# Optimization experiments

Measured on AMD Instinct MI355X. Metric: run time of the kernel, lower is better.

The kernel has to match this reference:

```python
import jax, jax.numpy as jnp
import numpy as np

N, IN_DIM, OUT_DIM, HEADS = 2048, 512, 512, 8
HEAD_DIM = OUT_DIM // HEADS
NEG_SLOPE = 0.2


def setup_inputs() -> dict:
    key = jax.random.key(0)
    k1, k2, k3, k4 = jax.random.split(key, 4)
    x = jax.random.normal(k1, (N, IN_DIM), dtype=jnp.float32)
    adj = jax.random.randint(k2, (N, N), 0, 2, dtype=jnp.int32)
    W = jax.random.normal(k3, (IN_DIM, OUT_DIM), dtype=jnp.float32) * 0.02
    a = jax.random.normal(k4, (2 * HEAD_DIM,), dtype=jnp.float32) * 0.02
    return {"x": x, "adj": adj, "W": W, "a": a}


def reference(x, adj, W, a):
    # Wh: (N, H, Dh)
    Wh = (x @ W).reshape(N, HEADS, HEAD_DIM)
    # a . concat(Wh_i, Wh_j) == (Wh_i . a_src) + (Wh_j . a_dst) -- exact decomposition,
    # avoids materializing the (N, N, H, 2*Dh) concat tensor.
    a_src, a_dst = a[:HEAD_DIM], a[HEAD_DIM:]
    s_i = jnp.einsum('nhd,d->nh', Wh, a_src)  # contribution of dest node i
    s_j = jnp.einsum('nhd,d->nh', Wh, a_dst)  # contribution of source node j
    e = jax.nn.leaky_relu(s_i[:, None, :] + s_j[None, :, :], negative_slope=NEG_SLOPE)  # (N, N, H)
    mask = (adj > 0)[:, :, None]
    e = jnp.where(mask, e, jnp.float32(-jnp.inf))
    alpha = jax.nn.softmax(e, axis=1)  # softmax over source nodes j
    # out[i,h,:] = sum_j alpha[i,j,h] * Wh[j,h,:]   (dropout is identity at eval)
    out = jnp.einsum('ijh,jhd->ihd', alpha, Wh)
    return out.reshape(N, OUT_DIM)
```

## Files before the change

kernel.cpp:

```cpp
#include <hip/hip_runtime.h>
#include <hip/hip_bf16.h>

#define NN 2048
#define KD 512
#define ODIM 512
#define NHEAD 8
#define HD 64
#define NEG 0.2f

typedef float f32x4 __attribute__((ext_vector_type(4)));
typedef short bf16x8 __attribute__((ext_vector_type(8)));
typedef short bf16x4 __attribute__((ext_vector_type(4)));
typedef unsigned long long u64;
typedef unsigned int u32;

__device__ __forceinline__ short tob(float f) {
  __hip_bfloat16 h = __float2bfloat16(f);
  return *reinterpret_cast<short*>(&h);
}

__device__ __forceinline__ void gl_lds16(const void* g, void* l) {
  __builtin_amdgcn_global_load_lds(
      (const __attribute__((address_space(1))) u32*)g,
      (__attribute__((address_space(3))) u32*)l, 16, 0, 0);
}
__device__ __forceinline__ void gl_lds4(const void* g, void* l) {
  __builtin_amdgcn_global_load_lds(
      (const __attribute__((address_space(1))) u32*)g,
      (__attribute__((address_space(3))) u32*)l, 4, 0, 0);
}

__global__ __launch_bounds__(256) void prep(const float* __restrict__ X,
                                            const float* __restrict__ W,
                                            const int* __restrict__ adj,
                                            short* __restrict__ Xf,
                                            short* __restrict__ Bf,
                                            unsigned short* __restrict__ bits) {
  __shared__ float sbuf[16 * 516];
  const int b = blockIdx.x;
  const int t = threadIdx.x;

  if (b < 1024) {
    const int T = b * 256 + t;
    const int row = T >> 7, g = T & 127;
    const int* p = adj + (size_t)row * NN + g * 16;
    u32 m = 0;
#pragma unroll
    for (int q = 0; q < 4; ++q) {
      const int4 v = *(const int4*)&p[q * 4];
      m |= (v.x > 0 ? 1u : 0u) << (q * 4);
      m |= (v.y > 0 ? 2u : 0u) << (q * 4);
      m |= (v.z > 0 ? 4u : 0u) << (q * 4);
      m |= (v.w > 0 ? 8u : 0u) << (q * 4);
    }
    bits[T] = (unsigned short)m;
    return;
  }

  if (b < 1024 + 128) {
    const int xb = b - 1024;
#pragma unroll
    for (int q = 0; q < 8; ++q) {
      const int flat = q * 256 + t;
      const int row = flat >> 7, c4 = flat & 127;
      const float4 v = *(const float4*)&X[(size_t)(xb * 16 + row) * KD + c4 * 4];
      *(float4*)&sbuf[row * 516 + c4 * 4] = v;
    }
    __syncthreads();
#pragma unroll
    for (int c = 0; c < 4; ++c) {
      const int s = c * 256 + t;
      const int ks = s >> 6, l = s & 63;
      const int col = l & 15, kg = (l >> 4) & 3;
      const int k0 = ks * 32 + kg * 8;
      bf16x8 o;
#pragma unroll
      for (int u = 0; u < 8; ++u) o[u] = tob(sbuf[col * 516 + k0 + u]);
      *(bf16x8*)&Xf[((size_t)xb * 1024 + s) * 8] = o;
    }
    return;
  }

  const int b2 = b - 1152;
  const int kb = b2 & 7, h = b2 >> 3;
  const int k0 = kb * 64;
#pragma unroll
  for (int q = 0; q < 4; ++q) {
    const int flat = q * 256 + t;
    const int kk = flat >> 4, o4 = (flat & 15) * 4;
    const float4 v = *(const float4*)&W[(size_t)(k0 + kk) * ODIM + h * 64 + o4];
    *(float4*)&sbuf[kk * 68 + o4] = v;
  }
  __syncthreads();
#pragma unroll
  for (int c = 0; c < 2; ++c) {
    const int s = c * 256 + t;
    const int ksl = s >> 8, nt = (s >> 6) & 3, l = s & 63;
    const int col = l & 15, kg = (l >> 4) & 3;
    const int kloc = ksl * 32 + kg * 8;
    const int od = nt * 16 + col;
    bf16x8 o;
#pragma unroll
    for (int u = 0; u < 8; ++u) o[u] = tob(sbuf[(kloc + u) * 68 + od]);
    const size_t off = (((size_t)(h * 4 + nt) * 16 + kb * 2 + ksl) * 64 + l) * 8;
    *(bf16x8*)&Bf[off] = o;
  }
}

__global__ __launch_bounds__(256) void gemm_fused(
    const short* __restrict__ Xf, const short* __restrict__ Bf,
    const float* __restrict__ a, short* __restrict__ WhF,
    float2* __restrict__ esrcp, u32* __restrict__ edstp) {
  const int t = threadIdx.x;
  const int lane = t & 63, w = t >> 6;
  const int col = lane & 15, kgrp = lane >> 4;
  const int bm = blockIdx.x * 64;
  const int h = blockIdx.y;
  const int mt = blockIdx.x * 4 + w;

  const short* ax = Xf + (size_t)mt * 8192;
  const short* bx = Bf + (size_t)h * 32768;

  f32x4 acc[4] = {};

#pragma unroll
  for (int ks = 0; ks < 16; ++ks) {
    const bf16x8 af = *(const bf16x8*)&ax[(ks * 64 + lane) * 8];
#pragma unroll
    for (int nt = 0; nt < 4; ++nt) {
      const bf16x8 bf = *(const bf16x8*)&bx[((nt * 16 + ks) * 64 + lane) * 8];
      acc[nt] = __builtin_amdgcn_mfma_f32_16x16x32_bf16(af, bf, acc[nt], 0, 0, 0);
    }
  }

  float asv[4], adv[4];
#pragma unroll
  for (int nt = 0; nt < 4; ++nt) {
    asv[nt] = a[nt * 16 + col];
    adv[nt] = a[64 + nt * 16 + col];
  }
  float ps[4], pd[4];
#pragma unroll
  for (int r = 0; r < 4; ++r) {
    float s1 = 0.f, s2 = 0.f;
#pragma unroll
    for (int nt = 0; nt < 4; ++nt) {
      s1 += acc[nt][r] * asv[nt];
      s2 += acc[nt][r] * adv[nt];
    }
    ps[r] = s1;
    pd[r] = s2;
  }
#pragma unroll
  for (int off = 1; off <= 8; off <<= 1) {
#pragma unroll
    for (int r = 0; r < 4; ++r) {
      ps[r] += __shfl_xor(ps[r], off);
      pd[r] += __shfl_xor(pd[r], off);
    }
  }
  {
    const size_t tbase = ((size_t)h * 32 + blockIdx.x) * 4096;
    const int lp = ((w & 1) * 2 + (kgrp >> 1)) * 16 + col;
    const int u0 = (kgrp & 1) * 4;
    const int slot_ks = w >> 1;
#pragma unroll
    for (int nt = 0; nt < 4; ++nt) {
      bf16x4 o;
#pragma unroll
      for (int r = 0; r < 4; ++r) o[r] = tob(acc[nt][r]);
      *(bf16x4*)&WhF[tbase + (size_t)(nt * 2 + slot_ks) * 512 + lp * 8 + u0] = o;
    }
  }
  if (col == 0) {
    const int mbase = bm + w * 16 + kgrp * 4;
#pragma unroll
    for (int r = 0; r < 4; ++r) {
      const int n = mbase + r;
      esrcp[h * NN + n] = make_float2(__expf(ps[r]), __expf(NEG * ps[r]));
      const u32 lo = (u32)(unsigned short)tob(__expf(pd[r]));
      const u32 hi = (u32)(unsigned short)tob(__expf(NEG * pd[r]));
      edstp[h * NN + n] = (hi << 16) | lo;
    }
  }
}

__global__ __launch_bounds__(256) void attn_mfma(
    const short* __restrict__ WhF, const unsigned char* __restrict__ adjbits,
    const float2* __restrict__ esrcp, const u32* __restrict__ edstp,
    float* __restrict__ out) {
  extern __shared__ __align__(16) char smem[];
  const int t = threadIdx.x;
  const int lane = t & 63;
  const int jq = t >> 6;
  const int col = lane & 15, kgrp = lane >> 4;
  const int h = blockIdx.y;
  const int i0 = blockIdx.x * 32;
  char* wbase = smem + jq * 17408;

  const short* tb = WhF + ((size_t)h * 32 + jq * 8) * 4096;
  const int jb = jq * 512;
  const int jboff = jb >> 3;

  const float2 e0 = esrcp[h * NN + i0 + col];
  const float2 e1 = esrcp[h * NN + i0 + 16 + col];
  const float A0 = e0.x, C0 = e0.y, A1 = e1.x, C1 = e1.y;

  bf16x8 ones;
#pragma unroll
  for (int u = 0; u < 8; ++u) ones[u] = (short)0x3F80;

  f32x4 acc[2][4] = {};
  f32x4 accd[2] = {};

  {
    char* bb = wbase;
#pragma unroll
    for (int s = 0; s < 8; ++s)
      gl_lds16(tb + s * 512 + lane * 8, bb + s * 1024);
    gl_lds4(edstp + h * NN + jb + lane, bb + 8192);
    gl_lds4(adjbits + (size_t)(i0 + (lane >> 1)) * 256 + jboff + (lane & 1) * 4,
            bb + 8448);
  }

#pragma unroll
  for (int tt = 0; tt < 8; ++tt) {
    char* bcur = wbase + (tt & 1) * 8704;
    char* bnxt = wbase + ((tt + 1) & 1) * 8704;
    if (tt < 7) {
      const short* g = tb + (size_t)(tt + 1) * 4096;
#pragma unroll
      for (int s = 0; s < 8; ++s)
        gl_lds16(g + s * 512 + lane * 8, bnxt + s * 1024);
      gl_lds4(edstp + h * NN + jb + (tt + 1) * 64 + lane, bnxt + 8192);
      gl_lds4(adjbits + (size_t)(i0 + (lane >> 1)) * 256 + jboff +
                  (tt + 1) * 8 + (lane & 1) * 4,
              bnxt + 8448);
      asm volatile("s_waitcnt vmcnt(10)" ::: "memory");
    } else {
      asm volatile("s_waitcnt vmcnt(0)" ::: "memory");
    }
    __builtin_amdgcn_sched_barrier(0);

    const u32* elds = (const u32*)(bcur + 8192);
    const u64 m0 = *(const u64*)(bcur + 8448 + col * 8);
    const u64 m1 = *(const u64*)(bcur + 8448 + 128 + col * 8);
    bf16x8 af0[2], af1[2];
#pragma unroll
    for (int ks = 0; ks < 2; ++ks) {
      const uint4 q0 = *(const uint4*)&elds[ks * 32 + kgrp * 8];
      const uint4 q1 = *(const uint4*)&elds[ks * 32 + kgrp * 8 + 4];
      const u32 mb0 = (u32)(m0 >> ((ks * 4 + kgrp) * 8)) & 0xffu;
      const u32 mb1 = (u32)(m1 >> ((ks * 4 + kgrp) * 8)) & 0xffu;
      const u32 uw[8] = {q0.x, q0.y, q0.z, q0.w, q1.x, q1.y, q1.z, q1.w};
#pragma unroll
      for (int u2 = 0; u2 < 8; ++u2) {
        const float B = __uint_as_float(uw[u2] << 16);
        const float D = __uint_as_float(uw[u2] & 0xffff0000u);
        float p0 = fmaxf(A0 * B, C0 * D);
        float p1 = fmaxf(A1 * B, C1 * D);
        p0 = ((mb0 >> u2) & 1u) ? p0 : 0.f;
        p1 = ((mb1 >> u2) & 1u) ? p1 : 0.f;
        af0[ks][u2] = tob(p0);
        af1[ks][u2] = tob(p1);
      }
    }

    const short* sb = (const short*)bcur;
    __builtin_amdgcn_s_setprio(1);
    accd[0] = __builtin_amdgcn_mfma_f32_16x16x32_bf16(af0[0], ones, accd[0], 0, 0, 0);
    accd[0] = __builtin_amdgcn_mfma_f32_16x16x32_bf16(af0[1], ones, accd[0], 0, 0, 0);
    accd[1] = __builtin_amdgcn_mfma_f32_16x16x32_bf16(af1[0], ones, accd[1], 0, 0, 0);
    accd[1] = __builtin_amdgcn_mfma_f32_16x16x32_bf16(af1[1], ones, accd[1], 0, 0, 0);
#pragma unroll
    for (int nt = 0; nt < 4; ++nt) {
      const bf16x8 b0 = *(const bf16x8*)&sb[(nt * 2 + 0) * 512 + lane * 8];
      const bf16x8 b1 = *(const bf16x8*)&sb[(nt * 2 + 1) * 512 + lane * 8];
      acc[0][nt] = __builtin_amdgcn_mfma_f32_16x16x32_bf16(af0[0], b0, acc[0][nt], 0, 0, 0);
      acc[1][nt] = __builtin_amdgcn_mfma_f32_16x16x32_bf16(af1[0], b0, acc[1][nt], 0, 0, 0);
      acc[0][nt] = __builtin_amdgcn_mfma_f32_16x16x32_bf16(af0[1], b1, acc[0][nt], 0, 0, 0);
      acc[1][nt] = __builtin_amdgcn_mfma_f32_16x16x32_bf16(af1[1], b1, acc[1][nt], 0, 0, 0);
    }
    __builtin_amdgcn_s_setprio(0);
  }

  __syncthreads();
  float* red = (float*)smem;
  float* rw = red + (size_t)jq * 32 * 66;
#pragma unroll
  for (int mt = 0; mt < 2; ++mt) {
#pragma unroll
    for (int nt = 0; nt < 4; ++nt)
#pragma unroll
      for (int r = 0; r < 4; ++r)
        rw[(mt * 16 + kgrp * 4 + r) * 66 + nt * 16 + col] = acc[mt][nt][r];
    if (col == 0) {
#pragma unroll
      for (int r = 0; r < 4; ++r)
        rw[(mt * 16 + kgrp * 4 + r) * 66 + 64] = accd[mt][r];
    }
  }
  __syncthreads();

  const int d = t & 63, rl = t >> 6;
#pragma unroll
  for (int rr = 0; rr < 8; ++rr) {
    const int row = rr * 4 + rl;
    float v = 0.f, dd = 0.f;
#pragma unroll
    for (int q = 0; q < 4; ++q) {
      v += red[((size_t)q * 32 + row) * 66 + d];
      dd += red[((size_t)q * 32 + row) * 66 + 64];
    }
    out[(size_t)(i0 + row) * ODIM + h * HD + d] = v / dd;
  }
}

extern "C" void kernel_launch(void* const* d_in, const int* in_sizes, int n_in,
                              void* d_out, int out_size, void* d_ws,
                              size_t ws_size, hipStream_t stream) {
  const float* x = (const float*)d_in[0];
  const int* adj = (const int*)d_in[1];
  const float* W = (const float*)d_in[2];
  const float* a = (const float*)d_in[3];
  float* out = (float*)d_out;

  char* ws = (char*)d_ws;
  short* WhF = (short*)ws;
  short* Xf = (short*)(ws + (2 << 20));
  short* Bf = (short*)(ws + (4 << 20));
  unsigned short* bits =
      (unsigned short*)(ws + (4 << 20) + (512 << 10));
  float2* esrcp = (float2*)(ws + (5 << 20));
  u32* edstp = (u32*)(ws + (5 << 20) + (128 << 10));

  prep<<<1216, 256, 0, stream>>>(x, W, adj, Xf, Bf, bits);
  gemm_fused<<<dim3(32, 8), 256, 0, stream>>>(Xf, Bf, a, WhF, esrcp, edstp);
  attn_mfma<<<dim3(64, 8), 256, 69632, stream>>>(
      WhF, (const unsigned char*)bits, esrcp, edstp, out);
}
```

Baseline: 37.31 us.

## Split attention over source-node chunks into partial kernel plus reduction kernel

Attention is restructured so each 512-thread block handles one head, 128 destination rows and one quarter of the source nodes. The whole Wh chunk is loaded into LDS once and shared by eight waves, each wave owning 16 rows, with adjacency bits read straight into registers. Partial numerators and denominators go to global workspace, and a separate reduce kernel sums the four quarters and normalizes. This adds grid parallelism and per-block reuse of Wh, at the cost of an extra launch, a partial-sum round-trip through memory, and loss of the old double-buffered load pipeline.

```diff
diff --git a/kernel.cpp b/kernel.cpp
--- a/kernel.cpp
+++ b/kernel.cpp
@@ -23,11 +23,6 @@
   __builtin_amdgcn_global_load_lds(
       (const __attribute__((address_space(1))) u32*)g,
       (__attribute__((address_space(3))) u32*)l, 16, 0, 0);
-}
-__device__ __forceinline__ void gl_lds4(const void* g, void* l) {
-  __builtin_amdgcn_global_load_lds(
-      (const __attribute__((address_space(1))) u32*)g,
-      (__attribute__((address_space(3))) u32*)l, 4, 0, 0);
 }
 
 __global__ __launch_bounds__(256) void prep(const float* __restrict__ X,
@@ -70,9 +65,9 @@
 #pragma unroll
     for (int c = 0; c < 4; ++c) {
       const int s = c * 256 + t;
-      const int ks = s >> 6, l = s & 63;
+      const int l = s & 63;
       const int col = l & 15, kg = (l >> 4) & 3;
-      const int k0 = ks * 32 + kg * 8;
+      const int k0 = (s >> 6) * 32 + kg * 8;
       bf16x8 o;
 #pragma unroll
       for (int u = 0; u < 8; ++u) o[u] = tob(sbuf[col * 516 + k0 + u]);
@@ -185,135 +180,127 @@
   }
 }
 
-__global__ __launch_bounds__(256) void attn_mfma(
+__global__ __launch_bounds__(512, 4) void attn_partial(
     const short* __restrict__ WhF, const unsigned char* __restrict__ adjbits,
     const float2* __restrict__ esrcp, const u32* __restrict__ edstp,
-    float* __restrict__ out) {
+    float* __restrict__ Pnum, float* __restrict__ Pden) {
   extern __shared__ __align__(16) char smem[];
   const int t = threadIdx.x;
   const int lane = t & 63;
-  const int jq = t >> 6;
+  const int wid = t >> 6;
   const int col = lane & 15, kgrp = lane >> 4;
+  const int ic = blockIdx.x;
   const int h = blockIdx.y;
-  const int i0 = blockIdx.x * 32;
-  char* wbase = smem + jq * 17408;
-
-  const short* tb = WhF + ((size_t)h * 32 + jq * 8) * 4096;
-  const int jb = jq * 512;
-  const int jboff = jb >> 3;
-
-  const float2 e0 = esrcp[h * NN + i0 + col];
-  const float2 e1 = esrcp[h * NN + i0 + 16 + col];
-  const float A0 = e0.x, C0 = e0.y, A1 = e1.x, C1 = e1.y;
+  const int jq = blockIdx.z;
+  const int i0w = ic * 128 + wid * 16;
+
+  {
+    const short* g = WhF + ((size_t)(h * 32 + jq * 8 + wid)) * 4096;
+#pragma unroll
+    for (int s = 0; s < 8; ++s)
+      gl_lds16(g + s * 512 + lane * 8, smem + (wid * 8 + s) * 1024);
+    if (wid == 0) {
+#pragma unroll
+      for (int d = 0; d < 2; ++d)
+        gl_lds16(edstp + h * NN + jq * 512 + d * 256 + lane * 4,
+                 smem + 65536 + d * 1024);
+    }
+  }
+  u64 aw[8];
+  {
+    const unsigned char* rb =
+        adjbits + (size_t)(i0w + col) * (NN / 8) + jq * 64;
+#pragma unroll
+    for (int q = 0; q < 4; ++q) {
+      const uint4 v = *(const uint4*)(rb + q * 16);
+      aw[q * 2] = (u64)v.x | ((u64)v.y << 32);
+      aw[q * 2 + 1] = (u64)v.z | ((u64)v.w << 32);
+    }
+  }
+  const float2 e0 = esrcp[h * NN + i0w + col];
+  const float A0 = e0.x, C0 = e0.y;
 
   bf16x8 ones;
 #pragma unroll
   for (int u = 0; u < 8; ++u) ones[u] = (short)0x3F80;
 
-  f32x4 acc[2][4] = {};
-  f32x4 accd[2] = {};
-
-  {
-    char* bb = wbase;
-#pragma unroll
-    for (int s = 0; s < 8; ++s)
-      gl_lds16(tb + s * 512 + lane * 8, bb + s * 1024);
-    gl_lds4(edstp + h * NN + jb + lane, bb + 8192);
-    gl_lds4(adjbits + (size_t)(i0 + (lane >> 1)) * 256 + jboff + (lane & 1) * 4,
-            bb + 8448);
-  }
-
-#pragma unroll
-  for (int tt = 0; tt < 8; ++tt) {
-    char* bcur = wbase + (tt & 1) * 8704;
-    char* bnxt = wbase + ((tt + 1) & 1) * 8704;
-    if (tt < 7) {
-      const short* g = tb + (size_t)(tt + 1) * 4096;
-#pragma unroll
-      for (int s = 0; s < 8; ++s)
-        gl_lds16(g + s * 512 + lane * 8, bnxt + s * 1024);
-      gl_lds4(edstp + h * NN + jb + (tt + 1) * 64 + lane, bnxt + 8192);
-      gl_lds4(adjbits + (size_t)(i0 + (lane >> 1)) * 256 + jboff +
-                  (tt + 1) * 8 + (lane & 1) * 4,
-              bnxt + 8448);
-      asm volatile("s_waitcnt vmcnt(10)" ::: "memory");
-    } else {
-      asm volatile("s_waitcnt vmcnt(0)" ::: "memory");
-    }
-    __builtin_amdgcn_sched_barrier(0);
-
-    const u32* elds = (const u32*)(bcur + 8192);
-    const u64 m0 = *(const u64*)(bcur + 8448 + col * 8);
-    const u64 m1 = *(const u64*)(bcur + 8448 + 128 + col * 8);
-    bf16x8 af0[2], af1[2];
+  __syncthreads();
+
+  f32x4 acc[4] = {};
+  f32x4 accd = {};
+  const u32* elds = (const u32*)(smem + 65536);
+
+#pragma unroll
+  for (int jt = 0; jt < 8; ++jt) {
+    const short* sb = (const short*)(smem + jt * 8192);
+    bf16x8 af[2];
 #pragma unroll
     for (int ks = 0; ks < 2; ++ks) {
-      const uint4 q0 = *(const uint4*)&elds[ks * 32 + kgrp * 8];
-      const uint4 q1 = *(const uint4*)&elds[ks * 32 + kgrp * 8 + 4];
-      const u32 mb0 = (u32)(m0 >> ((ks * 4 + kgrp) * 8)) & 0xffu;
-      const u32 mb1 = (u32)(m1 >> ((ks * 4 + kgrp) * 8)) & 0xffu;
+      const uint4 q0 = *(const uint4*)&elds[jt * 64 + ks * 32 + kgrp * 8];
+      const uint4 q1 = *(const uint4*)&elds[jt * 64 + ks * 32 + kgrp * 8 + 4];
+      const u32 mb = (u32)(aw[jt] >> ((ks * 4 + kgrp) * 8)) & 0xffu;
       const u32 uw[8] = {q0.x, q0.y, q0.z, q0.w, q1.x, q1.y, q1.z, q1.w};
 #pragma unroll
       for (int u2 = 0; u2 < 8; ++u2) {
         const float B = __uint_as_float(uw[u2] << 16);
         const float D = __uint_as_float(uw[u2] & 0xffff0000u);
-        float p0 = fmaxf(A0 * B, C0 * D);
-        float p1 = fmaxf(A1 * B, C1 * D);
-        p0 = ((mb0 >> u2) & 1u) ? p0 : 0.f;
-        p1 = ((mb1 >> u2) & 1u) ? p1 : 0.f;
-        af0[ks][u2] = tob(p0);
-        af1[ks][u2] = tob(p1);
+        float p = fmaxf(A0 * B, C0 * D);
+        p = ((mb >> u2) & 1u) ? p : 0.f;
+        af[ks][u2] = tob(p);
       }
     }
-
-    const short* sb = (const short*)bcur;
-    __builtin_amdgcn_s_setprio(1);
-    accd[0] = __builtin_amdgcn_mfma_f32_16x16x32_bf16(af0[0], ones, accd[0], 0, 0, 0);
-    accd[0] = __builtin_amdgcn_mfma_f32_16x16x32_bf16(af0[1], ones, accd[0], 0, 0, 0);
-    accd[1] = __builtin_amdgcn_mfma_f32_16x16x32_bf16(af1[0], ones, accd[1], 0, 0, 0);
-    accd[1] = __builtin_amdgcn_mfma_f32_16x16x32_bf16(af1[1], ones, accd[1], 0, 0, 0);
+    accd = __builtin_amdgcn_mfma_f32_16x16x32_bf16(af[0], ones, accd, 0, 0, 0);
+    accd = __builtin_amdgcn_mfma_f32_16x16x32_bf16(af[1], ones, accd, 0, 0, 0);
 #pragma unroll
     for (int nt = 0; nt < 4; ++nt) {
       const bf16x8 b0 = *(const bf16x8*)&sb[(nt * 2 + 0) * 512 + lane * 8];
       const bf16x8 b1 = *(const bf16x8*)&sb[(nt * 2 + 1) * 512 + lane * 8];
-      acc[0][nt] = __builtin_amdgcn_mfma_f32_16x16x32_bf16(af0[0], b0, acc[0][nt], 0, 0, 0);
-      acc[1][nt] = __builtin_amdgcn_mfma_f32_16x16x32_bf16(af1[0], b0, acc[1][nt], 0, 0, 0);
-      acc[0][nt] = __builtin_amdgcn_mfma_f32_16x16x32_bf16(af0[1], b1, acc[0][nt], 0, 0, 0);
-      acc[1][nt] = __builtin_amdgcn_mfma_f32_16x16x32_bf16(af1[1], b1, acc[1][nt], 0, 0, 0);
-    }
-    __builtin_amdgcn_s_setprio(0);
-  }
-
+      acc[nt] = __builtin_amdgcn_mfma_f32_16x16x32_bf16(af[0], b0, acc[nt], 0, 0, 0);
+      acc[nt] = __builtin_amdgcn_mfma_f32_16x16x32_bf16(af[1], b1, acc[nt], 0, 0, 0);
+    }
+  }
+
+  const int itg = ic * 8 + wid;
+  const size_t pb = (((size_t)(jq * 8 + h) * 128 + itg) * 4) * 256;
+#pragma unroll
+  for (int nt = 0; nt < 4; ++nt)
+    *(f32x4*)&Pnum[pb + (size_t)nt * 256 + lane * 4] = acc[nt];
+  if (col == 0) {
+    *(f32x4*)&Pden[(((size_t)(jq * 8 + h) * 128 + itg) * 16) + kgrp * 4] = accd;
+  }
+}
+
+__global__ __launch_bounds__(256) void reduce(const float* __restrict__ Pnum,
+                                              const float* __restrict__ Pden,
+                                              float* __restrict__ out) {
+  __shared__ float lds[16][68];
+  const int t = threadIdx.x;
+  const int it = blockIdx.x & 127, h = blockIdx.x >> 7;
+  const int nt = t >> 6, l = t & 63;
+  const int col = l & 15, kgrp = l >> 4;
+
+  f32x4 s = {};
+  f32x4 dd = {};
+#pragma unroll
+  for (int jq = 0; jq < 4; ++jq) {
+    const size_t pb = (((size_t)(jq * 8 + h) * 128 + it) * 4) * 256;
+    const f32x4 v = *(const f32x4*)&Pnum[pb + (size_t)nt * 256 + l * 4];
+    const f32x4 d =
+        *(const f32x4*)&Pden[(((size_t)(jq * 8 + h) * 128 + it) * 16) + kgrp * 4];
+#pragma unroll
+    for (int r = 0; r < 4; ++r) {
+      s[r] += v[r];
+      dd[r] += d[r];
+    }
+  }
+#pragma unroll
+  for (int r = 0; r < 4; ++r) lds[kgrp * 4 + r][nt * 16 + col] = s[r] / dd[r];
   __syncthreads();
-  float* red = (float*)smem;
-  float* rw = red + (size_t)jq * 32 * 66;
-#pragma unroll
-  for (int mt = 0; mt < 2; ++mt) {
-#pragma unroll
-    for (int nt = 0; nt < 4; ++nt)
-#pragma unroll
-      for (int r = 0; r < 4; ++r)
-        rw[(mt * 16 + kgrp * 4 + r) * 66 + nt * 16 + col] = acc[mt][nt][r];
-    if (col == 0) {
-#pragma unroll
-      for (int r = 0; r < 4; ++r)
-        rw[(mt * 16 + kgrp * 4 + r) * 66 + 64] = accd[mt][r];
-    }
-  }
-  __syncthreads();
-
-  const int d = t & 63, rl = t >> 6;
-#pragma unroll
-  for (int rr = 0; rr < 8; ++rr) {
-    const int row = rr * 4 + rl;
-    float v = 0.f, dd = 0.f;
-#pragma unroll
-    for (int q = 0; q < 4; ++q) {
-      v += red[((size_t)q * 32 + row) * 66 + d];
-      dd += red[((size_t)q * 32 + row) * 66 + 64];
-    }
-    out[(size_t)(i0 + row) * ODIM + h * HD + d] = v / dd;
-  }
+
+  const int row = t >> 4, q = t & 15;
+  const float4 o = *(const float4*)&lds[row][q * 4];
+  out[(size_t)(it * 16 + row) * ODIM + h * HD + q * 4] = o.x;
+  *(float4*)&out[(size_t)(it * 16 + row) * ODIM + h * HD + q * 4] = o;
 }
 
 extern "C" void kernel_launch(void* const* d_in, const int* in_sizes, int n_in,
@@ -333,9 +320,12 @@
       (unsigned short*)(ws + (4 << 20) + (512 << 10));
   float2* esrcp = (float2*)(ws + (5 << 20));
   u32* edstp = (u32*)(ws + (5 << 20) + (128 << 10));
+  float* Pnum = (float*)(ws + (6 << 20));
+  float* Pden = (float*)(ws + (23 << 20));
 
   prep<<<1216, 256, 0, stream>>>(x, W, adj, Xf, Bf, bits);
   gemm_fused<<<dim3(32, 8), 256, 0, stream>>>(Xf, Bf, a, WhF, esrcp, edstp);
-  attn_mfma<<<dim3(64, 8), 256, 69632, stream>>>(
-      WhF, (const unsigned char*)bits, esrcp, edstp, out);
-}
+  attn_partial<<<dim3(16, 8, 4), 512, 67584, stream>>>(
+      WhF, (const unsigned char*)bits, esrcp, edstp, Pnum, Pden);
+  reduce<<<1024, 256, 0, stream>>>(Pnum, Pden, out);
+}
```

New measurement: 40.91 us. 1.1x slower.
